# Kernel tuning notes

Measured on AMD Instinct MI355X. Metric: run time of the kernel, lower is better.

The kernel has to match this reference:

```python
import jax, jax.numpy as jnp
import numpy as np

LOG_SCALE_INIT = float(np.log(10.0))


def lorentz_linear(x, W, b, log_scale):
    # nonlin (gelu) -> linear -> Lorentz time/space renormalization
    y = jax.nn.gelu(x) @ W.T + b
    time = jax.nn.sigmoid(y[..., :1]) * jnp.exp(log_scale) + 1.1
    nar = y[..., 1:]
    denom = jnp.clip(jnp.sum(nar * nar, axis=-1, keepdims=True), 1e-8, None)
    scale = (time * time - 1.0) / denom
    return jnp.concatenate([time, nar * jnp.sqrt(scale)], axis=-1)


def ffn_lorentz(x, W1, b1, s1, W2, b2, s2):
    return lorentz_linear(lorentz_linear(x, W1, b1, s1), W2, b2, s2) + x


def knn_indices(x, k):
    # x: (B,N,C). KNN on detached features (as in ViG dense_knn_matrix).
    xs = jax.lax.stop_gradient(x)
    sq = jnp.sum(xs * xs, axis=-1)  # (B,N)
    d = sq[:, :, None] + sq[:, None, :] - 2.0 * jnp.einsum('bnc,bmc->bnm', xs, xs)
    _, idx = jax.lax.top_k(-d, k)  # (B,N,k) nearest (includes self)
    return idx


def graph_conv(x, Wg, bg, sg, k):
    # Max-relative graph conv with Lorentz linear. x: (B,N,C)
    idx = knn_indices(x, k)
    xj = jax.vmap(lambda xb, ib: xb[ib])(x, idx)  # (B,N,k,C) gather
    msg = jnp.max(xj - x[:, :, None, :], axis=2)  # (B,N,C)
    h = jnp.concatenate([x, msg], axis=-1)        # (B,N,2C)
    return lorentz_linear(h, Wg, bg, sg)


def setup_inputs() -> dict:
    key = jax.random.key(0)
    ks = jax.random.split(key, 8)
    B, C, H, W = 8, 192, 56, 56
    x = jax.random.normal(ks[0], (B, C, H, W), dtype=jnp.float32)
    def lin(k_, fin, fout):
        return jax.random.normal(k_, (fout, fin), dtype=jnp.float32) * 0.02
    p = {
        'x': x,
        'W1': lin(ks[1], C, C), 'b1': jnp.zeros((C,), jnp.float32), 's1': jnp.float32(LOG_SCALE_INIT),
        'W2': lin(ks[2], C, C), 'b2': jnp.zeros((C,), jnp.float32), 's2': jnp.float32(LOG_SCALE_INIT),
        'Wg': lin(ks[3], 2 * C, C), 'bg': jnp.zeros((C,), jnp.float32), 'sg': jnp.float32(LOG_SCALE_INIT),
        'W3': lin(ks[4], C, C), 'b3': jnp.zeros((C,), jnp.float32), 's3': jnp.float32(LOG_SCALE_INIT),
        'W4': lin(ks[5], C, C), 'b4': jnp.zeros((C,), jnp.float32), 's4': jnp.float32(LOG_SCALE_INIT),
        'k': 9,
    }
    return p


def reference(x, W1, b1, s1, W2, b2, s2, Wg, bg, sg, W3, b3, s3, W4, b4, s4, k):
    B, C, H, W = x.shape
    xn = x.reshape(B, C, H * W).transpose(0, 2, 1)  # (B,N,C) == rearrange b c (h w) 1 -> b (h w) c
    shortcut = xn
    xn = ffn_lorentz(xn, W1, b1, s1, W2, b2, s2)
    xn = graph_conv(xn, Wg, bg, sg, k)
    xn = ffn_lorentz(xn, W3, b3, s3, W4, b4, s4)
    xn = xn + shortcut  # drop_path = 0 -> identity
    return xn.transpose(0, 2, 1).reshape(B, C, H, W)
```

## Files before the change

kernel.cpp:

```cpp
#include <hip/hip_runtime.h>
#include <math.h>

#define NB   8
#define NC   192
#define NPIX 3136
#define NPAD 3200
#define NMT  98
#define GRID_LL (NB*NMT)
#define NIT  25
#define NSP  8
#define GRID_KNN (NB*NIT*NSP)
#define GRID_MSG (NB*196)
#define FINF 3.4e38f

typedef _Float16 f16x8 __attribute__((ext_vector_type(8)));
typedef float   f32x16 __attribute__((ext_vector_type(16)));

__device__ __forceinline__ float gelu_f(float x){
    float u = 0.7978845608028654f * (x + 0.044715f * x * x * x);
    return 0.5f * x * (1.0f + tanhf(u));
}
__device__ __forceinline__ unsigned short h2u(_Float16 v){
    union { _Float16 f; unsigned short u; } c; c.f = v; return c.u;
}
__device__ __forceinline__ unsigned pack_hi(float a, float b){
    return (unsigned)h2u((_Float16)a) | ((unsigned)h2u((_Float16)b) << 16);
}

#define LESS9(da,ia,db,ib) ((da) < (db) || ((da) == (db) && (ia) < (ib)))
#define CSW9(a,ia,b,ib) { bool sw_ = LESS9(b,ib,a,ia); float tf_=(a); int ti_=(ia); \
    (a) = sw_? (b) : (a); (ia) = sw_? (ib) : (ia); (b) = sw_? tf_ : (b); (ib) = sw_? ti_ : (ib); }

struct Top9 {
    float d0,d1,d2,d3,d4,d5,d6,d7,d8;
    int   j0,j1,j2,j3,j4,j5,j6,j7,j8;
    __device__ __forceinline__ void init(){
        d0=d1=d2=d3=d4=d5=d6=d7=d8=FINF;
        j0=j1=j2=j3=j4=j5=j6=j7=j8=0x7FFFFFFF;
    }
    __device__ __forceinline__ void insert(float nd, int ni){
        if (!LESS9(nd, ni, d8, j8)) return;
        d8 = nd; j8 = ni;
        CSW9(d7,j7,d8,j8); CSW9(d6,j6,d7,j7); CSW9(d5,j5,d6,j6); CSW9(d4,j4,d5,j5);
        CSW9(d3,j3,d4,j4); CSW9(d2,j2,d3,j3); CSW9(d1,j1,d2,j2); CSW9(d0,j0,d1,j1);
    }
};

__device__ __forceinline__ unsigned f2mono(float e){
    unsigned u = __float_as_uint(e);
    return u ^ ((unsigned)((int)u >> 31) | 0x80000000u);
}
__device__ __forceinline__ float unmono(unsigned m){
    return __uint_as_float(m ^ ((unsigned)(((int)~m) >> 31) | 0x80000000u));
}

#define CSK(a,b) { unsigned h_ = (a) > (b) ? (a) : (b); unsigned l_ = (a) > (b) ? (b) : (a); (a) = h_; (b) = l_; }
#define INSKEY(x_) if ((x_) > t_k11){ t_k11 = (x_); \
    CSK(t_k10,t_k11) CSK(t_k9,t_k10) CSK(t_k8,t_k9) CSK(t_k7,t_k8) \
    CSK(t_k6,t_k7) CSK(t_k5,t_k6) CSK(t_k4,t_k5) CSK(t_k3,t_k4) \
    CSK(t_k2,t_k3) CSK(t_k1,t_k2) CSK(t_k0,t_k1) }

#define KQ(A,Q) { \
    unsigned q0_ = (f2mono(A[4*(Q)+0]) & 0xFFFFF000u) | (unsigned)(jinvb_ - 8*(Q)    ); \
    unsigned q1_ = (f2mono(A[4*(Q)+1]) & 0xFFFFF000u) | (unsigned)(jinvb_ - 8*(Q) - 1); \
    unsigned q2_ = (f2mono(A[4*(Q)+2]) & 0xFFFFF000u) | (unsigned)(jinvb_ - 8*(Q) - 2); \
    unsigned q3_ = (f2mono(A[4*(Q)+3]) & 0xFFFFF000u) | (unsigned)(jinvb_ - 8*(Q) - 3); \
    unsigned qa_ = q0_ > q1_ ? q0_ : q1_; \
    unsigned qb_ = q2_ > q3_ ? q2_ : q3_; \
    unsigned qm_ = qa_ > qb_ ? qa_ : qb_; \
    if (qm_ > t_k11){ INSKEY(q0_) INSKEY(q1_) INSKEY(q2_) INSKEY(q3_) } }

#define AMAX16(A) fmaxf(fmaxf(fmaxf(fmaxf(A[0],A[1]),fmaxf(A[2],A[3])),fmaxf(fmaxf(A[4],A[5]),fmaxf(A[6],A[7]))), \
                        fmaxf(fmaxf(fmaxf(A[8],A[9]),fmaxf(A[10],A[11])),fmaxf(fmaxf(A[12],A[13]),fmaxf(A[14],A[15]))))

#define INSACCK(A,JS) { float am_ = AMAX16(A); \
    if (am_ >= thrf){ int jinvb_ = 4095 - (jg + (JS)*32 + 4*h); \
        KQ(A,0) KQ(A,1) KQ(A,2) KQ(A,3) } }

#define MF(ACC,AO,BO) ACC = __builtin_amdgcn_mfma_f32_32x32x16_f16(AO,BO,ACC,0,0,0);
#define ZERO16 {0,0,0,0,0,0,0,0,0,0,0,0,0,0,0,0}

__global__ __launch_bounds__(256) void wt_kernel(
    const float* __restrict__ W1, const float* __restrict__ W2,
    float* __restrict__ W1T, float* __restrict__ W2T)
{
    __shared__ float tile[32*33];
    int t = blockIdx.x;
    const float* src; float* dst;
    if (t < 36){ src = W1; dst = W1T; } else { src = W2; dst = W2T; t -= 36; }
    int tr = t / 6, tc = t - tr*6;
    int tid = threadIdx.x;
    {
        int i = tid >> 3, j4 = (tid & 7)*4;
        float4 v = *(const float4*)&src[(size_t)(tr*32 + i)*192 + tc*32 + j4];
        tile[i*33 + j4+0] = v.x; tile[i*33 + j4+1] = v.y;
        tile[i*33 + j4+2] = v.z; tile[i*33 + j4+3] = v.w;
    }
    __syncthreads();
    {
        int j = tid >> 3, i4 = (tid & 7)*4;
        float4 o = make_float4(tile[(i4+0)*33 + j], tile[(i4+1)*33 + j],
                               tile[(i4+2)*33 + j], tile[(i4+3)*33 + j]);
        *(float4*)&dst[(size_t)(tc*32 + j)*192 + tr*32 + i4] = o;
    }
}

__global__ __launch_bounds__(256) void wt16_kernel(
    const float* __restrict__ Wg, const float* __restrict__ W3,
    const float* __restrict__ W4,
    unsigned short* __restrict__ Wh, unsigned short* __restrict__ Wl)
{
    int i = blockIdx.x*256 + threadIdx.x;
    if (i >= 147456) return;
    const float* src; int off;
    if (i < 73728)       { src = Wg; off = i; }
    else if (i < 110592) { src = W3; off = i - 73728; }
    else                 { src = W4; off = i - 110592; }
    float w = src[off];
    _Float16 hi = (_Float16)w;
    Wh[i] = h2u(hi);
    Wl[i] = h2u((_Float16)(w - (float)hi));
}

__global__ __launch_bounds__(256) void pad_kernel(
    unsigned short* __restrict__ Xh, unsigned short* __restrict__ S2h)
{
    const int b = blockIdx.x;
    const int tid = threadIdx.x;
    uint4 z = make_uint4(0,0,0,0);
    for (int e = tid; e < 1536; e += 256){
        int r = e / 24, c8 = (e % 24) * 8;
        *(uint4*)&Xh[((size_t)b*NPAD + NPIX + r)*192 + c8] = z;
    }
    if (tid < 64){
        union { _Float16 f; unsigned short u; } p;
        p.f = (_Float16)(-30000.0f);
        S2h[(size_t)b*NPAD + NPIX + tid] = p.u;
    }
}

template<int K, bool WCM, bool DUAL, bool AX, bool CONVF>
__global__ __launch_bounds__(256, 4) void ll2_kernel(
    const float* __restrict__ A0, const float* __restrict__ A1,
    const float* __restrict__ WT, const float* __restrict__ bias,
    const float* __restrict__ sptr, const float* __restrict__ Xres,
    float* __restrict__ OutCM, float* __restrict__ Hrm,
    unsigned short* __restrict__ Xh, unsigned short* __restrict__ S2h,
    float* __restrict__ SQf)
{
    __shared__ float lA[32*36];
    __shared__ float lW[32*196];

    const int tid = threadIdx.x;
    const int tx = tid & 15, ty = tid >> 4;
    const int bid = blockIdx.x;
    const int b  = bid / NMT;
    const int n0 = (bid % NMT) * 32;

    float acc[2][12];
    #pragma unroll
    for (int mi = 0; mi < 2; ++mi)
        #pragma unroll
        for (int j = 0; j < 12; ++j) acc[mi][j] = 0.f;

    for (int kt = 0; kt < K/32; ++kt){
        {
            int kk = tid >> 3;
            int m4 = (tid & 7) * 4;
            int c  = kt*32 + kk;
            const float* pl;
            if (K > 192 && c >= 192) pl = A1 + ((size_t)b*192 + (c - 192))*NPIX;
            else                     pl = A0 + ((size_t)b*192 + c)*NPIX;
            float4 v = *(const float4*)&pl[n0 + m4];
            v.x = gelu_f(v.x); v.y = gelu_f(v.y); v.z = gelu_f(v.z); v.w = gelu_f(v.w);
            *(float4*)&lA[kk*36 + m4] = v;
        }
        #pragma unroll
        for (int r = 0; r < 6; ++r){
            int e  = tid + r*256;
            int kk = e / 48;
            int c4 = (e - kk*48) * 4;
            float4 v = *(const float4*)&WT[(size_t)(kt*32 + kk)*192 + c4];
            *(float4*)&lW[kk*196 + c4] = v;
        }
        __syncthreads();
        #pragma unroll
        for (int kk = 0; kk < 32; ++kk){
            float2 a2 = *(const float2*)&lA[kk*36 + ty*2];
            float4 w0 = *(const float4*)&lW[kk*196 + tx*12];
            float4 w1 = *(const float4*)&lW[kk*196 + tx*12 + 4];
            float4 w2 = *(const float4*)&lW[kk*196 + tx*12 + 8];
            float aw[2]  = {a2.x, a2.y};
            float wv[12] = {w0.x,w0.y,w0.z,w0.w, w1.x,w1.y,w1.z,w1.w, w2.x,w2.y,w2.z,w2.w};
            #pragma unroll
            for (int mi = 0; mi < 2; ++mi)
                #pragma unroll
                for (int j = 0; j < 12; ++j)
                    acc[mi][j] = fmaf(aw[mi], wv[j], acc[mi][j]);
        }
        __syncthreads();
    }

    const int lane = tid & 63;
    float es = expf(sptr[0]);
    float bv[12];
    #pragma unroll
    for (int q = 0; q < 3; ++q){
        float4 t4 = *(const float4*)&bias[tx*12 + q*4];
        bv[q*4+0] = t4.x; bv[q*4+1] = t4.y; bv[q*4+2] = t4.z; bv[q*4+3] = t4.w;
    }
    #pragma unroll
    for (int mi = 0; mi < 2; ++mi){
        float part = 0.f;
        #pragma unroll
        for (int j = 0; j < 12; ++j){
            float y = acc[mi][j] + bv[j];
            acc[mi][j] = y;
            if (!(tx == 0 && j == 0)) part += y * y;
        }
        #pragma unroll
        for (int m = 1; m < 16; m <<= 1) part += __shfl_xor(part, m, 64);
        float y0   = __shfl(acc[mi][0], lane & 48, 64);
        float tval = es / (1.f + expf(-y0)) + 1.1f;
        float denom = fmaxf(part, 1e-8f);
        float sca  = (tval*tval - 1.f) / denom;
        float sqs  = sqrtf(sca);
        #pragma unroll
        for (int j = 0; j < 12; ++j){
            float o = acc[mi][j] * sqs;
            if (tx == 0 && j == 0) o = tval;
            acc[mi][j] = o;
        }
    }
    if (AX){
        #pragma unroll
        for (int j = 0; j < 12; ++j){
            int c = tx*12 + j;
            float2 xv = *(const float2*)&Xres[((size_t)b*192 + c)*NPIX + n0 + ty*2];
            acc[0][j] += xv.x; acc[1][j] += xv.y;
        }
    }
    if (WCM){
        #pragma unroll
        for (int j = 0; j < 12; ++j){
            int c = tx*12 + j;
            *(float2*)&OutCM[((size_t)b*192 + c)*NPIX + n0 + ty*2] = make_float2(acc[0][j], acc[1][j]);
        }
    }
    if (DUAL){
        #pragma unroll
        for (int mi = 0; mi < 2; ++mi){
            #pragma unroll
            for (int q = 0; q < 3; ++q){
                float4 o = make_float4(acc[mi][q*4+0], acc[mi][q*4+1], acc[mi][q*4+2], acc[mi][q*4+3]);
                *(float4*)&Hrm[((size_t)b*NPIX + n0 + ty*2 + mi)*192 + tx*12 + q*4] = o;
            }
        }
    }
    if (CONVF){
        #pragma unroll
        for (int mi = 0; mi < 2; ++mi){
            int row = n0 + ty*2 + mi;
            float s = 0.f;
            #pragma unroll
            for (int j = 0; j < 12; ++j) s = fmaf(acc[mi][j], acc[mi][j], s);
            #pragma unroll
            for (int m = 1; m < 16; m <<= 1) s += __shfl_xor(s, m, 64);
            #pragma unroll
            for (int q = 0; q < 3; ++q){
                uint2 hv;
                hv.x = pack_hi(acc[mi][q*4+0], acc[mi][q*4+1]);
                hv.y = pack_hi(acc[mi][q*4+2], acc[mi][q*4+3]);
                *(uint2*)&Xh[((size_t)b*NPAD + row)*192 + tx*12 + q*4] = hv;
            }
            if (tx == 0){
                SQf[(size_t)b*NPIX + row] = s;
                S2h[(size_t)b*NPAD + row] = h2u((_Float16)(-0.5f * s));
            }
        }
    }
}

template<int K, int AMODE, bool ESPL, bool EF32, bool AXCM, bool ARRM, bool OUTCM>
__global__ __launch_bounds__(192) void mll_kernel(
    const unsigned short* __restrict__ Ash, const unsigned short* __restrict__ Asl,
    const float* __restrict__ Af0, const float* __restrict__ Af1,
    const unsigned short* __restrict__ Wh, const unsigned short* __restrict__ Wl,
    const float* __restrict__ bias, const float* __restrict__ sptr,
    const float* __restrict__ Xcm, const float* __restrict__ Rrm,
    float* __restrict__ OutF,
    unsigned short* __restrict__ Oh, unsigned short* __restrict__ Ol)
{
    __shared__ float psum[3][32], y0v[32];
    const int tid = threadIdx.x;
    const int w = tid >> 6, lane = tid & 63, l31 = lane & 31, h = lane >> 5;
    const int bid = blockIdx.x;
    const int b = bid / NMT, mt = bid % NMT;
    const int row0 = mt*32;
    const int nb = w*64;
    const size_t arow = (size_t)b*NPIX + row0 + l31;
    const int c0 = nb + l31, c1 = nb + 32 + l31;

    f32x16 acc0 = ZERO16, acc1 = ZERO16;

    #pragma unroll
    for (int ks = 0; ks < K/16; ++ks){
        const int kb = ks*16 + h*8;
        f16x8 ah, al;
        if (AMODE == 0){
            ah = __builtin_bit_cast(f16x8, *(const uint4*)&Ash[arow*192 + kb]);
            al = __builtin_bit_cast(f16x8, *(const uint4*)&Asl[arow*192 + kb]);
        } else {
            const float* src;
            if (AMODE == 2) src = (ks < 12) ? (Af0 + arow*192 + kb) : (Af1 + arow*192 + (kb - 192));
            else            src = Af0 + arow*192 + kb;
            float4 f0 = *(const float4*)src;
            float4 f1 = *(const float4*)(src + 4);
            float g[8] = {f0.x,f0.y,f0.z,f0.w,f1.x,f1.y,f1.z,f1.w};
            #pragma unroll
            for (int e = 0; e < 8; ++e){
                float gg = gelu_f(g[e]);
                _Float16 hi = (_Float16)gg;
                ah[e] = hi;
                al[e] = (_Float16)(gg - (float)hi);
            }
        }
        f16x8 wh0 = __builtin_bit_cast(f16x8, *(const uint4*)&Wh[(size_t)c0*K + kb]);
        f16x8 wl0 = __builtin_bit_cast(f16x8, *(const uint4*)&Wl[(size_t)c0*K + kb]);
        f16x8 wh1 = __builtin_bit_cast(f16x8, *(const uint4*)&Wh[(size_t)c1*K + kb]);
        f16x8 wl1 = __builtin_bit_cast(f16x8, *(const uint4*)&Wl[(size_t)c1*K + kb]);
        MF(acc0, ah, wh0) MF(acc0, al, wh0) MF(acc0, ah, wl0)
        MF(acc1, ah, wh1) MF(acc1, al, wh1) MF(acc1, ah, wl1)
    }

    const float es = expf(sptr[0]);
    const float bv0 = bias[c0], bv1 = bias[c1];
    float o0[16], o1[16], p[16];
    #pragma unroll
    for (int r = 0; r < 16; ++r){
        o0[r] = acc0[r] + bv0;
        o1[r] = acc1[r] + bv1;
        p[r] = o0[r]*o0[r] + o1[r]*o1[r];
    }
    #pragma unroll
    for (int m = 1; m < 32; m <<= 1){
        #pragma unroll
        for (int r = 0; r < 16; ++r) p[r] += __shfl_xor(p[r], m, 64);
    }
    if (l31 == 0){
        #pragma unroll
        for (int r = 0; r < 16; ++r){
            int row = (r&3) + 8*(r>>2) + 4*h;
            float v = p[r];
            if (w == 0){ v -= o0[r]*o0[r]; y0v[row] = o0[r]; }
            psum[w][row] = v;
        }
    }
    __syncthreads();
    #pragma unroll
    for (int r = 0; r < 16; ++r){
        int row = (r&3) + 8*(r>>2) + 4*h;
        float S = psum[0][row] + psum[1][row] + psum[2][row];
        float y0 = y0v[row];
        float tval = es / (1.f + expf(-y0)) + 1.1f;
        float denom = fmaxf(S, 1e-8f);
        float sqs = sqrtf((tval*tval - 1.f)/denom);
        o0[r] *= sqs; o1[r] *= sqs;
        if (w == 0 && l31 == 0) o0[r] = tval;
    }
    if (AXCM){
        #pragma unroll
        for (int p4 = 0; p4 < 4; ++p4){
            float4 xv0 = *(const float4*)&Xcm[((size_t)b*192 + c0)*NPIX + row0 + 8*p4 + 4*h];
            float4 xv1 = *(const float4*)&Xcm[((size_t)b*192 + c1)*NPIX + row0 + 8*p4 + 4*h];
            o0[4*p4+0] += xv0.x; o0[4*p4+1] += xv0.y; o0[4*p4+2] += xv0.z; o0[4*p4+3] += xv0.w;
            o1[4*p4+0] += xv1.x; o1[4*p4+1] += xv1.y; o1[4*p4+2] += xv1.z; o1[4*p4+3] += xv1.w;
        }
    }
    if (ARRM){
        #pragma unroll
        for (int r = 0; r < 16; ++r){
            int row = (r&3) + 8*(r>>2) + 4*h;
            o0[r] += Rrm[((size_t)b*NPIX + row0 + row)*192 + c0];
            o1[r] += Rrm[((size_t)b*NPIX + row0 + row)*192 + c1];
        }
    }
    if (OUTCM){
        #pragma unroll
        for (int p4 = 0; p4 < 4; ++p4){
            *(float4*)&OutF[((size_t)b*192 + c0)*NPIX + row0 + 8*p4 + 4*h] =
                make_float4(o0[4*p4+0], o0[4*p4+1], o0[4*p4+2], o0[4*p4+3]);
            *(float4*)&OutF[((size_t)b*192 + c1)*NPIX + row0 + 8*p4 + 4*h] =
                make_float4(o1[4*p4+0], o1[4*p4+1], o1[4*p4+2], o1[4*p4+3]);
        }
    }
    if (EF32){
        #pragma unroll
        for (int r = 0; r < 16; ++r){
            int row = (r&3) + 8*(r>>2) + 4*h;
            OutF[((size_t)b*NPIX + row0 + row)*192 + c0] = o0[r];
            OutF[((size_t)b*NPIX + row0 + row)*192 + c1] = o1[r];
        }
    }
    if (ESPL){
        #pragma unroll
        for (int r = 0; r < 16; ++r){
            int row = (r&3) + 8*(r>>2) + 4*h;
            size_t o = ((size_t)b*NPIX + row0 + row)*192;
            float g0 = gelu_f(o0[r]);
            _Float16 h0 = (_Float16)g0;
            Oh[o + c0] = h2u(h0);
            Ol[o + c0] = h2u((_Float16)(g0 - (float)h0));
            float g1 = gelu_f(o1[r]);
            _Float16 h1 = (_Float16)g1;
            Oh[o + c1] = h2u(h1);
            Ol[o + c1] = h2u((_Float16)(g1 - (float)h1));
        }
    }
}

__global__ __launch_bounds__(256) __attribute__((amdgpu_waves_per_eu(2))) void knn_kernel(
    const unsigned short* __restrict__ Xh, const unsigned short* __restrict__ S2h,
    unsigned* __restrict__ PK)
{
    __shared__ uint4 lds[2][640];

    const int tid  = threadIdx.x;
    const int lane = tid & 63;
    const int w    = tid >> 6;
    const int l31  = lane & 31;
    const int h    = lane >> 5;
    const int bid  = blockIdx.x;
    const int b    = bid & 7;
    const int t2   = bid >> 3;
    const int itile = t2 >> 3;
    const int sp    = t2 & 7;
    const int i0    = itile * 128;
    const int g0 = (sp*25)/NSP, g1 = ((sp+1)*25)/NSP;
    const size_t rowb = (size_t)b * NPAD;

    const size_t bbase = (rowb + i0 + w*32 + l31)*192;
    f16x8 B[6][2];
    #pragma unroll
    for (int kc = 0; kc < 6; ++kc)
        #pragma unroll
        for (int ks = 0; ks < 2; ++ks)
            B[kc][ks] = __builtin_bit_cast(f16x8, *(const uint4*)&Xh[bbase + kc*32 + (ks*2 + h)*8]);

    unsigned t_k0=0,t_k1=0,t_k2=0,t_k3=0,t_k4=0,t_k5=0,
             t_k6=0,t_k7=0,t_k8=0,t_k9=0,t_k10=0,t_k11=0;
    float thrf = -FINF;

    const int rs0 = tid >> 2, seg0 = tid & 3;
    const int wr0 = rs0*5 + seg0, wr1 = (rs0 + 64)*5 + seg0;

    uint4 pv0 = *(const uint4*)&Xh[(rowb + g0*128 + rs0)*192 + seg0*8];
    uint4 pv1 = *(const uint4*)&Xh[(rowb + g0*128 + rs0 + 64)*192 + seg0*8];

    for (int g = g0; g < g1; ++g){
        const int jg = g*128;
        f32x16 acc0 = ZERO16, acc1 = ZERO16, acc2 = ZERO16, acc3 = ZERO16;

        #pragma unroll
        for (int kc = 0; kc < 6; ++kc){
            const int buf = kc & 1;
            lds[buf][wr0] = pv0;
            lds[buf][wr1] = pv1;
            {
                int nkc = (kc < 5) ? kc + 1 : 0;
                int njg = (kc < 5) ? jg : jg + 128;
                if (kc < 5 || g + 1 < g1){
                    pv0 = *(const uint4*)&Xh[(rowb + njg + rs0)*192 + nkc*32 + seg0*8];
                    pv1 = *(const uint4*)&Xh[(rowb + njg + rs0 + 64)*192 + nkc*32 + seg0*8];
                }
            }
            __syncthreads();
            #pragma unroll
            for (int ks = 0; ks < 2; ++ks){
                int rb = l31*5 + (ks*2 + h);
                f16x8 bh = B[kc][ks];
                f16x8 a0h = __builtin_bit_cast(f16x8, lds[buf][  0 + rb]);
                f16x8 a1h = __builtin_bit_cast(f16x8, lds[buf][160 + rb]);
                f16x8 a2h = __builtin_bit_cast(f16x8, lds[buf][320 + rb]);
                f16x8 a3h = __builtin_bit_cast(f16x8, lds[buf][480 + rb]);
                MF(acc0, a0h, bh)
                MF(acc1, a1h, bh)
                MF(acc2, a2h, bh)
                MF(acc3, a3h, bh)
            }
        }

        {
            unsigned m  = (h == 0) ? 0xFFFFFFFFu : 0u;
            unsigned om = 0x3C00u & m;
            f16x8 one = __builtin_bit_cast(f16x8, make_uint4(om, 0, 0, 0));
            unsigned s0 = (unsigned)S2h[rowb + jg +  0 + l31];
            unsigned s1 = (unsigned)S2h[rowb + jg + 32 + l31];
            unsigned s2 = (unsigned)S2h[rowb + jg + 64 + l31];
            unsigned s3 = (unsigned)S2h[rowb + jg + 96 + l31];
            f16x8 a;
            a = __builtin_bit_cast(f16x8, make_uint4(s0 & m, 0,0,0)); MF(acc0, a, one)
            a = __builtin_bit_cast(f16x8, make_uint4(s1 & m, 0,0,0)); MF(acc1, a, one)
            a = __builtin_bit_cast(f16x8, make_uint4(s2 & m, 0,0,0)); MF(acc2, a, one)
            a = __builtin_bit_cast(f16x8, make_uint4(s3 & m, 0,0,0)); MF(acc3, a, one)
        }

        INSACCK(acc0, 0)
        INSACCK(acc1, 1)
        INSACCK(acc2, 2)
        INSACCK(acc3, 3)
        thrf = (t_k11 != 0u) ? unmono(t_k11 & 0xFFFFF000u) : -FINF;
    }

    #define MRGK(Kk) { unsigned ok_ = __shfl((int)(Kk), lane ^ 32, 64); \
                      if (lane < 32) { INSKEY((unsigned)ok_) } }
    MRGK(t_k0) MRGK(t_k1) MRGK(t_k2) MRGK(t_k3) MRGK(t_k4) MRGK(t_k5)
    MRGK(t_k6) MRGK(t_k7) MRGK(t_k8) MRGK(t_k9) MRGK(t_k10) MRGK(t_k11)

    if (lane < 32){
        size_t po = ((size_t)(t2*8 + b)*128 + (size_t)w*32 + l31)*12;
        PK[po+ 0] = t_k0;  PK[po+ 1] = t_k1;  PK[po+ 2] = t_k2;  PK[po+ 3] = t_k3;
        PK[po+ 4] = t_k4;  PK[po+ 5] = t_k5;  PK[po+ 6] = t_k6;  PK[po+ 7] = t_k7;
        PK[po+ 8] = t_k8;  PK[po+ 9] = t_k9;  PK[po+10] = t_k10; PK[po+11] = t_k11;
    }
}

__global__ __launch_bounds__(256) void merge_msg_kernel(
    const float* __restrict__ H, const float* __restrict__ SQf,
    const unsigned* __restrict__ PK, float* __restrict__ Msg)
{
    __shared__ float liX[16*196];
    __shared__ unsigned kv[1600];
    __shared__ float cd[256];
    __shared__ int   cidx[256];
    __shared__ int   fidx[144];

    const int tid = threadIdx.x;
    const int bid = blockIdx.x;
    const int b  = bid / 196;
    const int i0 = (bid % 196) * 16;
    const int base = b * NPIX;

    #pragma unroll
    for (int k = 0; k < 3; ++k){
        int f = tid + k*256;
        int r = f / 48, c4 = f % 48;
        *(float4*)&liX[r*196 + c4*4] = *(const float4*)&H[(size_t)(base + i0 + r)*192 + c4*4];
    }
    if (tid < 128){
        int r = tid >> 3, sp = tid & 7;
        int i = i0 + r;
        size_t po = ((size_t)(((i>>7)*NSP + sp)*8 + b)*128 + (i & 127))*12;
        #pragma unroll
        for (int q = 0; q < 3; ++q)
            *(uint4*)&kv[r*100 + sp*12 + q*4] = *(const uint4*)&PK[po + q*4];
    }
    __syncthreads();

    if (tid < 16){
        int r = tid;
        int h0=0,h1=0,h2=0,h3=0,h4=0,h5=0,h6=0,h7=0;
        #pragma unroll
        for (int p = 0; p < 16; ++p){
            unsigned bk = 0; int bs = 0;
#define HEADC(SP,HV) { \
            unsigned k_ = (HV < 12) ? kv[r*100 + SP*12 + HV] : 0u; \
            bool bt_ = k_ > bk; \
            bk = bt_? k_ : bk; bs = bt_? SP : bs; }
            HEADC(0,h0) HEADC(1,h1) HEADC(2,h2) HEADC(3,h3)
            HEADC(4,h4) HEADC(5,h5) HEADC(6,h6) HEADC(7,h7)
#undef HEADC
            cidx[r*16 + p] = 4095 - (int)(bk & 0xFFFu);
            h0 += (bs==0); h1 += (bs==1); h2 += (bs==2); h3 += (bs==3);
            h4 += (bs==4); h5 += (bs==5); h6 += (bs==6); h7 += (bs==7);
        }
    }
    __syncthreads();

    {
        int r = tid >> 4, p = tid & 15;
        int j = cidx[r*16 + p];
        const float* hj = &H[(size_t)(base + j)*192];
        float dot = 0.f;
        #pragma unroll
        for (int q = 0; q < 48; ++q){
            float4 xv = *(const float4*)&liX[r*196 + q*4];
            float4 yv = *(const float4*)&hj[q*4];
            dot = fmaf(xv.x,yv.x, fmaf(xv.y,yv.y, fmaf(xv.z,yv.z, fmaf(xv.w,yv.w, dot))));
        }
        cd[r*16 + p] = SQf[base + j] - 2.f*dot;
    }
    __syncthreads();

    if (tid < 16){
        int r = tid;
        Top9 m; m.init();
        #pragma unroll
        for (int c = 0; c < 16; ++c) m.insert(cd[r*16 + c], cidx[r*16 + c]);
        fidx[r*9+0]=m.j0; fidx[r*9+1]=m.j1; fidx[r*9+2]=m.j2; fidx[r*9+3]=m.j3;
        fidx[r*9+4]=m.j4; fidx[r*9+5]=m.j5; fidx[r*9+6]=m.j6; fidx[r*9+7]=m.j7;
        fidx[r*9+8]=m.j8;
    }
    __syncthreads();

    int rr = tid >> 4, part = tid & 15;
    int ii = i0 + rr;
    int nbr[9];
    #pragma unroll
    for (int e = 0; e < 9; ++e) nbr[e] = fidx[rr*9 + e];
    #pragma unroll
    for (int q = 0; q < 3; ++q){
        float4 mv = make_float4(-FINF, -FINF, -FINF, -FINF);
        #pragma unroll
        for (int e = 0; e < 9; ++e){
            float4 v = *(const float4*)&H[(size_t)(base + nbr[e])*192 + part*12 + q*4];
            mv.x = fmaxf(mv.x, v.x); mv.y = fmaxf(mv.y, v.y);
            mv.z = fmaxf(mv.z, v.z); mv.w = fmaxf(mv.w, v.w);
        }
        float4 xi = *(const float4*)&liX[rr*196 + part*12 + q*4];
        *(float4*)&Msg[(size_t)(base + ii)*192 + part*12 + q*4] =
            make_float4(mv.x - xi.x, mv.y - xi.y, mv.z - xi.z, mv.w - xi.w);
    }
}

extern "C" void kernel_launch(void* const* d_in, const int* in_sizes, int n_in,
                              void* d_out, int out_size, void* d_ws, size_t ws_size,
                              hipStream_t stream)
{
    const float* x  = (const float*)d_in[0];
    const float* W1 = (const float*)d_in[1];
    const float* b1 = (const float*)d_in[2];
    const float* s1 = (const float*)d_in[3];
    const float* W2 = (const float*)d_in[4];
    const float* b2 = (const float*)d_in[5];
    const float* s2 = (const float*)d_in[6];
    const float* Wg = (const float*)d_in[7];
    const float* bg = (const float*)d_in[8];
    const float* sg = (const float*)d_in[9];
    const float* W3 = (const float*)d_in[10];
    const float* b3 = (const float*)d_in[11];
    const float* s3 = (const float*)d_in[12];
    const float* W4 = (const float*)d_in[13];
    const float* b4 = (const float*)d_in[14];
    const float* s4 = (const float*)d_in[15];
    float* ws = (float*)d_ws;
    float* out = (float*)d_out;

    const size_t NE = (size_t)NB*NPIX*192;
    float* T1cm = ws;
    float* Msg  = ws;
    float* Hrm = ws + NE;
    unsigned short* GT3h = (unsigned short*)Hrm;
    unsigned short* GT3l = GT3h + NE;
    float* X2f = ws + 2*NE;
    unsigned short* Xh  = (unsigned short*)(ws + 3*NE);
    unsigned short* S2h = Xh + (size_t)NB*NPAD*192;
    float* SQf = (float*)(S2h + (size_t)NB*NPAD);
    unsigned* PK = (unsigned*)(SQf + (size_t)NB*NPIX);
    float* W1T = (float*)(PK + (size_t)GRID_KNN*128*12);
    float* W2T = W1T + 36864;
    unsigned short* Wh16 = (unsigned short*)(W2T + 36864);
    unsigned short* Wl16 = Wh16 + 147456;
    const unsigned short* Wgh = Wh16,          *Wgl = Wl16;
    const unsigned short* W3h = Wh16 + 73728,  *W3l = Wl16 + 73728;
    const unsigned short* W4h = Wh16 + 110592, *W4l = Wl16 + 110592;

    wt_kernel<<<72, 256, 0, stream>>>(W1, W2, W1T, W2T);
    wt16_kernel<<<576, 256, 0, stream>>>(Wg, W3, W4, Wh16, Wl16);
    pad_kernel<<<NB, 256, 0, stream>>>(Xh, S2h);
    ll2_kernel<192, true , false, false, false><<<GRID_LL, 256, 0, stream>>>(
        x, x, W1T, b1, s1, nullptr, T1cm, nullptr, nullptr, nullptr, nullptr);
    ll2_kernel<192, false, true , true , true ><<<GRID_LL, 256, 0, stream>>>(
        T1cm, T1cm, W2T, b2, s2, x, nullptr, Hrm, Xh, S2h, SQf);
    knn_kernel<<<GRID_KNN, 256, 0, stream>>>(Xh, S2h, PK);
    merge_msg_kernel<<<GRID_MSG, 256, 0, stream>>>(Hrm, SQf, PK, Msg);
    mll_kernel<384,2,false,true ,false,false,false><<<GRID_LL, 192, 0, stream>>>(
        nullptr, nullptr, Hrm, Msg, Wgh, Wgl, bg, sg, nullptr, nullptr,
        X2f, nullptr, nullptr);
    mll_kernel<192,1,true ,false,false,false,false><<<GRID_LL, 192, 0, stream>>>(
        nullptr, nullptr, X2f, nullptr, W3h, W3l, b3, s3, nullptr, nullptr,
        nullptr, GT3h, GT3l);
    mll_kernel<192,0,false,false,true ,true ,true ><<<GRID_LL, 192, 0, stream>>>(
        GT3h, GT3l, nullptr, nullptr, W4h, W4l, b4, s4, x, X2f,
        out, nullptr, nullptr);
}
```

Baseline: 425.3 us.

## Fuse graph-conv linear and second FFN into one kernel with LDS tiles

```diff
diff --git a/kernel.cpp b/kernel.cpp
--- a/kernel.cpp
+++ b/kernel.cpp
@@ -281,17 +281,53 @@
     }
 }
 
-template<int K, int AMODE, bool ESPL, bool EF32, bool AXCM, bool ARRM, bool OUTCM>
-__global__ __launch_bounds__(192) void mll_kernel(
-    const unsigned short* __restrict__ Ash, const unsigned short* __restrict__ Asl,
-    const float* __restrict__ Af0, const float* __restrict__ Af1,
-    const unsigned short* __restrict__ Wh, const unsigned short* __restrict__ Wl,
-    const float* __restrict__ bias, const float* __restrict__ sptr,
-    const float* __restrict__ Xcm, const float* __restrict__ Rrm,
-    float* __restrict__ OutF,
-    unsigned short* __restrict__ Oh, unsigned short* __restrict__ Ol)
+#define MLL_EPI(O0,O1,ACC0,ACC1,BIAS,SPTR) { \
+    const float es_ = expf((SPTR)[0]); \
+    const float bv0_ = (BIAS)[c0], bv1_ = (BIAS)[c1]; \
+    float p_[16]; \
+    _Pragma("unroll") for (int r = 0; r < 16; ++r){ \
+        O0[r] = ACC0[r] + bv0_; O1[r] = ACC1[r] + bv1_; \
+        p_[r] = O0[r]*O0[r] + O1[r]*O1[r]; } \
+    _Pragma("unroll") for (int m_ = 1; m_ < 32; m_ <<= 1){ \
+        _Pragma("unroll") for (int r = 0; r < 16; ++r) p_[r] += __shfl_xor(p_[r], m_, 64); } \
+    if (l31 == 0){ \
+        _Pragma("unroll") for (int r = 0; r < 16; ++r){ \
+            int row = (r&3) + 8*(r>>2) + 4*h; \
+            float v = p_[r]; \
+            if (w == 0){ v -= O0[r]*O0[r]; y0v[row] = O0[r]; } \
+            psum[w][row] = v; } } \
+    __syncthreads(); \
+    _Pragma("unroll") for (int r = 0; r < 16; ++r){ \
+        int row = (r&3) + 8*(r>>2) + 4*h; \
+        float S_ = psum[0][row] + psum[1][row] + psum[2][row]; \
+        float y0_ = y0v[row]; \
+        float tv_ = es_ / (1.f + expf(-y0_)) + 1.1f; \
+        float dn_ = fmaxf(S_, 1e-8f); \
+        float sq_ = sqrtf((tv_*tv_ - 1.f)/dn_); \
+        O0[r] *= sq_; O1[r] *= sq_; \
+        if (w == 0 && l31 == 0) O0[r] = tv_; } \
+    __syncthreads(); }
+
+#define GSPLIT8(SRC,AH,AL) { \
+    _Pragma("unroll") for (int e_ = 0; e_ < 8; ++e_){ \
+        float gg_ = gelu_f((SRC)[e_]); \
+        _Float16 hi_ = (_Float16)gg_; \
+        AH[e_] = hi_; AL[e_] = (_Float16)(gg_ - (float)hi_); } }
+
+__global__ __launch_bounds__(192) void mfuse_kernel(
+    const float* __restrict__ Hrm, const float* __restrict__ Msg,
+    const unsigned short* __restrict__ Wgh, const unsigned short* __restrict__ Wgl,
+    const unsigned short* __restrict__ W3h, const unsigned short* __restrict__ W3l,
+    const unsigned short* __restrict__ W4h, const unsigned short* __restrict__ W4l,
+    const float* __restrict__ bg, const float* __restrict__ sg,
+    const float* __restrict__ b3, const float* __restrict__ s3,
+    const float* __restrict__ b4, const float* __restrict__ s4,
+    const float* __restrict__ x, float* __restrict__ out)
 {
     __shared__ float psum[3][32], y0v[32];
+    __shared__ float tileA[32*198];
+    __shared__ float tileB[32*198];
+
     const int tid = threadIdx.x;
     const int w = tid >> 6, lane = tid & 63, l31 = lane & 31, h = lane >> 5;
     const int bid = blockIdx.x;
@@ -301,120 +337,100 @@
     const size_t arow = (size_t)b*NPIX + row0 + l31;
     const int c0 = nb + l31, c1 = nb + 32 + l31;
 
-    f32x16 acc0 = ZERO16, acc1 = ZERO16;
-
-    #pragma unroll
-    for (int ks = 0; ks < K/16; ++ks){
-        const int kb = ks*16 + h*8;
-        f16x8 ah, al;
-        if (AMODE == 0){
-            ah = __builtin_bit_cast(f16x8, *(const uint4*)&Ash[arow*192 + kb]);
-            al = __builtin_bit_cast(f16x8, *(const uint4*)&Asl[arow*192 + kb]);
-        } else {
-            const float* src;
-            if (AMODE == 2) src = (ks < 12) ? (Af0 + arow*192 + kb) : (Af1 + arow*192 + (kb - 192));
-            else            src = Af0 + arow*192 + kb;
-            float4 f0 = *(const float4*)src;
-            float4 f1 = *(const float4*)(src + 4);
-            float g[8] = {f0.x,f0.y,f0.z,f0.w,f1.x,f1.y,f1.z,f1.w};
-            #pragma unroll
-            for (int e = 0; e < 8; ++e){
-                float gg = gelu_f(g[e]);
-                _Float16 hi = (_Float16)gg;
-                ah[e] = hi;
-                al[e] = (_Float16)(gg - (float)hi);
-            }
-        }
-        f16x8 wh0 = __builtin_bit_cast(f16x8, *(const uint4*)&Wh[(size_t)c0*K + kb]);
-        f16x8 wl0 = __builtin_bit_cast(f16x8, *(const uint4*)&Wl[(size_t)c0*K + kb]);
-        f16x8 wh1 = __builtin_bit_cast(f16x8, *(const uint4*)&Wh[(size_t)c1*K + kb]);
-        f16x8 wl1 = __builtin_bit_cast(f16x8, *(const uint4*)&Wl[(size_t)c1*K + kb]);
-        MF(acc0, ah, wh0) MF(acc0, al, wh0) MF(acc0, ah, wl0)
-        MF(acc1, ah, wh1) MF(acc1, al, wh1) MF(acc1, ah, wl1)
-    }
-
-    const float es = expf(sptr[0]);
-    const float bv0 = bias[c0], bv1 = bias[c1];
-    float o0[16], o1[16], p[16];
-    #pragma unroll
-    for (int r = 0; r < 16; ++r){
-        o0[r] = acc0[r] + bv0;
-        o1[r] = acc1[r] + bv1;
-        p[r] = o0[r]*o0[r] + o1[r]*o1[r];
-    }
-    #pragma unroll
-    for (int m = 1; m < 32; m <<= 1){
-        #pragma unroll
-        for (int r = 0; r < 16; ++r) p[r] += __shfl_xor(p[r], m, 64);
-    }
-    if (l31 == 0){
+    float o0[16], o1[16];
+
+    {
+        f32x16 acc0 = ZERO16, acc1 = ZERO16;
+        #pragma unroll
+        for (int ks = 0; ks < 24; ++ks){
+            const int kb = ks*16 + h*8;
+            const float* src = (ks < 12) ? (Hrm + arow*192 + kb) : (Msg + arow*192 + (kb - 192));
+            float g[8];
+            *(float4*)&g[0] = *(const float4*)src;
+            *(float4*)&g[4] = *(const float4*)(src + 4);
+            f16x8 ah, al;
+            GSPLIT8(g, ah, al)
+            f16x8 wh0 = __builtin_bit_cast(f16x8, *(const uint4*)&Wgh[(size_t)c0*384 + kb]);
+            f16x8 wl0 = __builtin_bit_cast(f16x8, *(const uint4*)&Wgl[(size_t)c0*384 + kb]);
+            f16x8 wh1 = __builtin_bit_cast(f16x8, *(const uint4*)&Wgh[(size_t)c1*384 + kb]);
+            f16x8 wl1 = __builtin_bit_cast(f16x8, *(const uint4*)&Wgl[(size_t)c1*384 + kb]);
+            MF(acc0, ah, wh0) MF(acc0, al, wh0) MF(acc0, ah, wl0)
+            MF(acc1, ah, wh1) MF(acc1, al, wh1) MF(acc1, ah, wl1)
+        }
+        MLL_EPI(o0, o1, acc0, acc1, bg, sg)
         #pragma unroll
         for (int r = 0; r < 16; ++r){
             int row = (r&3) + 8*(r>>2) + 4*h;
-            float v = p[r];
-            if (w == 0){ v -= o0[r]*o0[r]; y0v[row] = o0[r]; }
-            psum[w][row] = v;
-        }
-    }
-    __syncthreads();
-    #pragma unroll
-    for (int r = 0; r < 16; ++r){
-        int row = (r&3) + 8*(r>>2) + 4*h;
-        float S = psum[0][row] + psum[1][row] + psum[2][row];
-        float y0 = y0v[row];
-        float tval = es / (1.f + expf(-y0)) + 1.1f;
-        float denom = fmaxf(S, 1e-8f);
-        float sqs = sqrtf((tval*tval - 1.f)/denom);
-        o0[r] *= sqs; o1[r] *= sqs;
-        if (w == 0 && l31 == 0) o0[r] = tval;
-    }
-    if (AXCM){
+            tileA[row*198 + c0] = o0[r];
+            tileA[row*198 + c1] = o1[r];
+        }
+        __syncthreads();
+    }
+
+    {
+        f32x16 acc0 = ZERO16, acc1 = ZERO16;
+        #pragma unroll
+        for (int ks = 0; ks < 12; ++ks){
+            const int kb = ks*16 + h*8;
+            float g[8];
+            #pragma unroll
+            for (int e = 0; e < 8; ++e) g[e] = tileA[l31*198 + kb + e];
+            f16x8 ah, al;
+            GSPLIT8(g, ah, al)
+            f16x8 wh0 = __builtin_bit_cast(f16x8, *(const uint4*)&W3h[(size_t)c0*192 + kb]);
+            f16x8 wl0 = __builtin_bit_cast(f16x8, *(const uint4*)&W3l[(size_t)c0*192 + kb]);
+            f16x8 wh1 = __builtin_bit_cast(f16x8, *(const uint4*)&W3h[(size_t)c1*192 + kb]);
+            f16x8 wl1 = __builtin_bit_cast(f16x8, *(const uint4*)&W3l[(size_t)c1*192 + kb]);
+            MF(acc0, ah, wh0) MF(acc0, al, wh0) MF(acc0, ah, wl0)
+            MF(acc1, ah, wh1) MF(acc1, al, wh1) MF(acc1, ah, wl1)
+        }
+        MLL_EPI(o0, o1, acc0, acc1, b3, s3)
+        #pragma unroll
+        for (int r = 0; r < 16; ++r){
+            int row = (r&3) + 8*(r>>2) + 4*h;
+            tileB[row*198 + c0] = o0[r];
+            tileB[row*198 + c1] = o1[r];
+        }
+        __syncthreads();
+    }
+
+    {
+        f32x16 acc0 = ZERO16, acc1 = ZERO16;
+        #pragma unroll
+        for (int ks = 0; ks < 12; ++ks){
+            const int kb = ks*16 + h*8;
+            float g[8];
+            #pragma unroll
+            for (int e = 0; e < 8; ++e) g[e] = tileB[l31*198 + kb + e];
+            f16x8 ah, al;
+            GSPLIT8(g, ah, al)
+            f16x8 wh0 = __builtin_bit_cast(f16x8, *(const uint4*)&W4h[(size_t)c0*192 + kb]);
+            f16x8 wl0 = __builtin_bit_cast(f16x8, *(const uint4*)&W4l[(size_t)c0*192 + kb]);
+            f16x8 wh1 = __builtin_bit_cast(f16x8, *(const uint4*)&W4h[(size_t)c1*192 + kb]);
+            f16x8 wl1 = __builtin_bit_cast(f16x8, *(const uint4*)&W4l[(size_t)c1*192 + kb]);
+            MF(acc0, ah, wh0) MF(acc0, al, wh0) MF(acc0, ah, wl0)
+            MF(acc1, ah, wh1) MF(acc1, al, wh1) MF(acc1, ah, wl1)
+        }
+        MLL_EPI(o0, o1, acc0, acc1, b4, s4)
+        #pragma unroll
+        for (int r = 0; r < 16; ++r){
+            int row = (r&3) + 8*(r>>2) + 4*h;
+            o0[r] += tileA[row*198 + c0];
+            o1[r] += tileA[row*198 + c1];
+        }
         #pragma unroll
         for (int p4 = 0; p4 < 4; ++p4){
-            float4 xv0 = *(const float4*)&Xcm[((size_t)b*192 + c0)*NPIX + row0 + 8*p4 + 4*h];
-            float4 xv1 = *(const float4*)&Xcm[((size_t)b*192 + c1)*NPIX + row0 + 8*p4 + 4*h];
+            float4 xv0 = *(const float4*)&x[((size_t)b*192 + c0)*NPIX + row0 + 8*p4 + 4*h];
+            float4 xv1 = *(const float4*)&x[((size_t)b*192 + c1)*NPIX + row0 + 8*p4 + 4*h];
             o0[4*p4+0] += xv0.x; o0[4*p4+1] += xv0.y; o0[4*p4+2] += xv0.z; o0[4*p4+3] += xv0.w;
             o1[4*p4+0] += xv1.x; o1[4*p4+1] += xv1.y; o1[4*p4+2] += xv1.z; o1[4*p4+3] += xv1.w;
         }
-    }
-    if (ARRM){
-        #pragma unroll
-        for (int r = 0; r < 16; ++r){
-            int row = (r&3) + 8*(r>>2) + 4*h;
-            o0[r] += Rrm[((size_t)b*NPIX + row0 + row)*192 + c0];
-            o1[r] += Rrm[((size_t)b*NPIX + row0 + row)*192 + c1];
-        }
-    }
-    if (OUTCM){
         #pragma unroll
         for (int p4 = 0; p4 < 4; ++p4){
-            *(float4*)&OutF[((size_t)b*192 + c0)*NPIX + row0 + 8*p4 + 4*h] =
+            *(float4*)&out[((size_t)b*192 + c0)*NPIX + row0 + 8*p4 + 4*h] =
                 make_float4(o0[4*p4+0], o0[4*p4+1], o0[4*p4+2], o0[4*p4+3]);
-            *(float4*)&OutF[((size_t)b*192 + c1)*NPIX + row0 + 8*p4 + 4*h] =
+            *(float4*)&out[((size_t)b*192 + c1)*NPIX + row0 + 8*p4 + 4*h] =
                 make_float4(o1[4*p4+0], o1[4*p4+1], o1[4*p4+2], o1[4*p4+3]);
-        }
-    }
-    if (EF32){
-        #pragma unroll
-        for (int r = 0; r < 16; ++r){
-            int row = (r&3) + 8*(r>>2) + 4*h;
-            OutF[((size_t)b*NPIX + row0 + row)*192 + c0] = o0[r];
-            OutF[((size_t)b*NPIX + row0 + row)*192 + c1] = o1[r];
-        }
-    }
-    if (ESPL){
-        #pragma unroll
-        for (int r = 0; r < 16; ++r){
-            int row = (r&3) + 8*(r>>2) + 4*h;
-            size_t o = ((size_t)b*NPIX + row0 + row)*192;
-            float g0 = gelu_f(o0[r]);
-            _Float16 h0 = (_Float16)g0;
-            Oh[o + c0] = h2u(h0);
-            Ol[o + c0] = h2u((_Float16)(g0 - (float)h0));
-            float g1 = gelu_f(o1[r]);
-            _Float16 h1 = (_Float16)g1;
-            Oh[o + c1] = h2u(h1);
-            Ol[o + c1] = h2u((_Float16)(g1 - (float)h1));
         }
     }
 }
@@ -649,10 +665,7 @@
     const size_t NE = (size_t)NB*NPIX*192;
     float* T1cm = ws;
     float* Msg  = ws;
-    float* Hrm = ws + NE;
-    unsigned short* GT3h = (unsigned short*)Hrm;
-    unsigned short* GT3l = GT3h + NE;
-    float* X2f = ws + 2*NE;
+    float* Hrm  = ws + NE;
     unsigned short* Xh  = (unsigned short*)(ws + 3*NE);
     unsigned short* S2h = Xh + (size_t)NB*NPAD*192;
     float* SQf = (float*)(S2h + (size_t)NB*NPAD);
@@ -674,13 +687,7 @@
         T1cm, T1cm, W2T, b2, s2, x, nullptr, Hrm, Xh, S2h, SQf);
     knn_kernel<<<GRID_KNN, 256, 0, stream>>>(Xh, S2h, PK);
     merge_msg_kernel<<<GRID_MSG, 256, 0, stream>>>(Hrm, SQf, PK, Msg);
-    mll_kernel<384,2,false,true ,false,false,false><<<GRID_LL, 192, 0, stream>>>(
-        nullptr, nullptr, Hrm, Msg, Wgh, Wgl, bg, sg, nullptr, nullptr,
-        X2f, nullptr, nullptr);
-    mll_kernel<192,1,true ,false,false,false,false><<<GRID_LL, 192, 0, stream>>>(
-        nullptr, nullptr, X2f, nullptr, W3h, W3l, b3, s3, nullptr, nullptr,
-        nullptr, GT3h, GT3l);
-    mll_kernel<192,0,false,false,true ,true ,true ><<<GRID_LL, 192, 0, stream>>>(
-        GT3h, GT3l, nullptr, nullptr, W4h, W4l, b4, s4, x, X2f,
-        out, nullptr, nullptr);
-}
+    mfuse_kernel<<<GRID_LL, 192, 0, stream>>>(
+        Hrm, Msg, Wgh, Wgl, W3h, W3l, W4h, W4l,
+        bg, sg, b3, s3, b4, s4, x, out);
+}
```

New measurement: 440.9 us. +3.7%, slower.
